# Kernel tuning notes

Hardware: AMD Instinct MI355X
Metric: run time of the kernel (lower is better)

Reference implementation:

```python
import jax, jax.numpy as jnp
import numpy as np

EPS = 1e-5
K = 20

def knn_idx(x, k):
    # x: (B, N, C). Torch computes -||xi-xj||^2 and takes topk (largest => nearest).
    xx = jnp.sum(x * x, axis=-1)                      # (B, N)
    inner = jnp.einsum('bnc,bmc->bnm', x, x)          # (B, N, N)
    neg_dist = 2.0 * inner - xx[:, :, None] - xx[:, None, :]
    return jax.lax.top_k(neg_dist, k)[1]              # (B, N, k) int32

def edge_feature(x, k):
    # x: (B, N, C) -> (B, N, k, 2C) = concat(neighbor - center, center)
    B = x.shape[0]
    idx = knn_idx(x, k)
    nb = x[jnp.arange(B)[:, None, None], idx]         # (B, N, k, C) gather
    ctr = jnp.broadcast_to(x[:, :, None, :], nb.shape)
    return jnp.concatenate([nb - ctr, ctr], axis=-1)

def batchnorm(x, gamma, beta, axes):
    # training-mode BN over `axes` (per-channel on last axis)
    m = jnp.mean(x, axis=axes, keepdims=True)
    v = jnp.var(x, axis=axes, keepdims=True)
    return (x - m) * jax.lax.rsqrt(v + EPS) * gamma + beta

def lrelu(x):
    return jnp.where(x >= 0, x, 0.2 * x)

def conv_bn_act(x, w, g, b):
    # 1x1 conv on (B, N, k, Cin) with weight (Cout, Cin), BN over (B, N, k)
    y = jnp.einsum('bnkc,oc->bnko', x, w)
    return lrelu(batchnorm(y, g, b, (0, 1, 2)))


def setup_inputs() -> dict:
    key = jax.random.key(0)
    ks = jax.random.split(key, 16)
    B, N = 4, 4096
    d = {'x': jax.random.normal(ks[0], (B, 3, N), dtype=jnp.float32)}
    d['w1'] = jax.random.normal(ks[1], (64, 6),    dtype=jnp.float32) * 0.1
    d['w2'] = jax.random.normal(ks[2], (64, 64),   dtype=jnp.float32) * 0.1
    d['w3'] = jax.random.normal(ks[3], (64, 128),  dtype=jnp.float32) * 0.1
    d['w4'] = jax.random.normal(ks[4], (64, 64),   dtype=jnp.float32) * 0.1
    d['w5'] = jax.random.normal(ks[5], (64, 128),  dtype=jnp.float32) * 0.1
    d['w6'] = jax.random.normal(ks[6], (1024, 192), dtype=jnp.float32) * 0.05
    d['wl'] = jax.random.normal(ks[7], (512, 1024), dtype=jnp.float32) * 0.05
    for i, c in zip(range(1, 8), [64, 64, 64, 64, 64, 1024, 512]):
        d[f'g{i}'] = jnp.ones((c,), jnp.float32)
        d[f'b{i}'] = jnp.zeros((c,), jnp.float32)
    return d


def reference(x, w1, w2, w3, w4, w5, w6, wl,
              g1, b1, g2, b2, g3, b3, g4, b4, g5, b5, g6, b6, g7, b7):
    p = jnp.transpose(x[:, :3, :], (0, 2, 1))         # (B, N, 3)
    # EdgeConv block 1
    e = edge_feature(p, K)                            # (B, N, k, 6)
    h = conv_bn_act(e, w1, g1, b1)
    h = conv_bn_act(h, w2, g2, b2)
    x1 = jnp.max(h, axis=2)                           # (B, N, 64)
    # EdgeConv block 2
    e = edge_feature(x1, K)                           # (B, N, k, 128)
    h = conv_bn_act(e, w3, g3, b3)
    h = conv_bn_act(h, w4, g4, b4)
    x2 = jnp.max(h, axis=2)
    # EdgeConv block 3
    e = edge_feature(x2, K)
    h = conv_bn_act(e, w5, g5, b5)
    x3 = jnp.max(h, axis=2)
    # point-wise 1x1 conv to 1024 then global max pool
    cat = jnp.concatenate([x1, x2, x3], axis=-1)      # (B, N, 192)
    h = lrelu(batchnorm(jnp.einsum('bnc,oc->bno', cat, w6), g6, b6, (0, 1)))
    g = jnp.max(h, axis=1)                            # (B, 1024)
    out = batchnorm(g @ wl.T, g7, b7, (0,))           # (B, 512)
    return out
```

## Files before the change

kernel.cpp:

```cpp
#include <hip/hip_runtime.h>

static constexpr int PB  = 4;
static constexpr int PN  = 4096;
static constexpr int PK  = 20;
static constexpr int PNT = PB*PN*PK;
#define NEGF (-3.402823466e38f)

__device__ __forceinline__ float lrelu_f(float x){ return x >= 0.f ? x : 0.2f*x; }

typedef __attribute__((ext_vector_type(8))) short short8v;
typedef __attribute__((ext_vector_type(4))) float f32x4;

__device__ __forceinline__ unsigned short f2bf(float f){
  unsigned u = __float_as_uint(f);
  unsigned r = u + 0x7FFFu + ((u>>16)&1u);
  return (unsigned short)(r>>16);
}
__device__ __forceinline__ float bf2f(unsigned short s){ return __uint_as_float(((unsigned)s)<<16); }

#define FMA4C(accv, av, bv) { accv = fmaf((av).x,(bv).x,accv); accv = fmaf((av).y,(bv).y,accv); \
                              accv = fmaf((av).z,(bv).z,accv); accv = fmaf((av).w,(bv).w,accv); }

__global__ __launch_bounds__(512) void k_knn3(const float* __restrict__ x, int* __restrict__ idxb){
  __shared__ float4 pts[PN];
  int t = threadIdx.x;
  int b = blockIdx.y;
  const float* xb = x + (size_t)b*3*PN;
  for(int i=t;i<PN;i+=512){
    float a0 = xb[i], a1 = xb[PN+i], a2 = xb[2*PN+i];
    float s = a0*a0; s = fmaf(a1,a1,s); s = fmaf(a2,a2,s);
    pts[i] = make_float4(a0,a1,a2,s);
  }
  __syncthreads();
  int lane = t & 63, w = t >> 6;
  int row = blockIdx.x*8 + w;
  float4 pi = pts[row];
  unsigned long long removed = 0ull;

#define KDIST(E) ({ float4 pj_ = pts[lane + ((E)<<6)]; \
    float dt_ = pi.x*pj_.x; dt_ = fmaf(pi.y,pj_.y,dt_); dt_ = fmaf(pi.z,pj_.z,dt_); \
    fmaf(2.f,dt_,-pi.w) - pj_.w; })

  float gv0,gv1,gv2,gv3,gv4,gv5,gv6,gv7;
  int   gi0,gi1,gi2,gi3,gi4,gi5,gi6,gi7;
#define KBUILDG(G) { float gm_=NEGF; int ge_=(G)*8; \
    _Pragma("unroll") for(int e_=(G)*8; e_<(G)*8+8; e_++){ \
      bool ok_ = ((removed >> e_) & 1ull) == 0ull; \
      float d_ = KDIST(e_); \
      bool bt_ = ok_ && (d_ > gm_); gm_ = bt_ ? d_ : gm_; ge_ = bt_ ? e_ : ge_; } \
    gv##G = gm_; gi##G = ge_; }
  KBUILDG(0) KBUILDG(1) KBUILDG(2) KBUILDG(3) KBUILDG(4) KBUILDG(5) KBUILDG(6) KBUILDG(7)

  float lmax; int le;
#define KLBEST { lmax = gv0; le = gi0; \
    if(gv1>lmax){lmax=gv1;le=gi1;} if(gv2>lmax){lmax=gv2;le=gi2;} \
    if(gv3>lmax){lmax=gv3;le=gi3;} if(gv4>lmax){lmax=gv4;le=gi4;} \
    if(gv5>lmax){lmax=gv5;le=gi5;} if(gv6>lmax){lmax=gv6;le=gi6;} \
    if(gv7>lmax){lmax=gv7;le=gi7;} }
  KLBEST

  int myidx = 0;
  for(int k=0;k<PK;k++){
    float g = lmax;
    #pragma unroll
    for(int s=32;s>=1;s>>=1) g = fmaxf(g, __shfl_xor(g, s));
    unsigned long long cand = __ballot(lmax == g);
    int jw;
    if(__popcll(cand) == 1){
      int wl = __ffsll(cand) - 1;
      int e  = __shfl(le, wl);
      jw = wl + (e<<6);
    } else {
      unsigned jj = (lmax == g) ? (unsigned)(lane + (le<<6)) : 0xFFFFFFFFu;
      #pragma unroll
      for(int s=32;s>=1;s>>=1){ unsigned o = __shfl_xor(jj, s); jj = (o < jj) ? o : jj; }
      jw = (int)jj;
    }
    if(lane == k) myidx = jw;
    if((jw & 63) == lane){
      int e = jw >> 6;
      removed |= (1ull << e);
      int q = e >> 3;
      if(q==0){ KBUILDG(0) } else if(q==1){ KBUILDG(1) }
      else if(q==2){ KBUILDG(2) } else if(q==3){ KBUILDG(3) }
      else if(q==4){ KBUILDG(4) } else if(q==5){ KBUILDG(5) }
      else if(q==6){ KBUILDG(6) } else { KBUILDG(7) }
      KLBEST
    }
  }
  if(lane < PK) idxb[((size_t)b*PN + row)*PK + lane] = myidx;
#undef KDIST
#undef KBUILDG
#undef KLBEST
}

__global__ __launch_bounds__(256) void k_dist64(const float* __restrict__ Xb, const float* __restrict__ xxb,
                                                float* __restrict__ D){
  __shared__ float Xi[128*32];
  __shared__ float Xj[128*32];
  __shared__ float xxi[128], xxj[128];
  int t = threadIdx.x;
  int p = blockIdx.x;
  int bi = (int)((65.0f - sqrtf(4225.0f - 8.0f*(float)p)) * 0.5f);
  while((bi+1)*32 - ((bi+1)*bi)/2 <= p) bi++;
  while(bi*32 - (bi*(bi-1))/2 > p) bi--;
  int bj = bi + (p - (bi*32 - (bi*(bi-1))/2));
  int i0 = bi*128, j0 = bj*128;
  int prg = t>>4, cq = t&15;
  float acc[8][8];
  #pragma unroll
  for(int pp=0;pp<8;pp++)
    #pragma unroll
    for(int oc=0;oc<8;oc++) acc[pp][oc] = 0.f;

  for(int h=0;h<2;h++){
    if(h) __syncthreads();
    #pragma unroll
    for(int k=0;k<4;k++){
      int fid = t + k*256; int row = fid>>3, c4 = fid&7;
      ((float4*)Xi)[row*8 + (c4^(row&7))] = ((const float4*)(Xb + (size_t)(i0+row)*64 + h*32))[c4];
      ((float4*)Xj)[row*8 + (c4^(row&7))] = ((const float4*)(Xb + (size_t)(j0+row)*64 + h*32))[c4];
    }
    if(h==0){
      if(t < 128) xxi[t] = xxb[i0+t];
      else        xxj[t-128] = xxb[j0+t-128];
    }
    __syncthreads();
    #pragma unroll 4
    for(int c4=0;c4<8;c4++){
      float4 a[8], bb[8];
      #pragma unroll
      for(int pp=0;pp<8;pp++){ int row = prg*8+pp; a[pp] = ((const float4*)Xi)[row*8 + (c4^(row&7))]; }
      #pragma unroll
      for(int oc=0;oc<8;oc++){ int col = cq+16*oc;  bb[oc] = ((const float4*)Xj)[col*8 + (c4^(col&7))]; }
      #pragma unroll
      for(int pp=0;pp<8;pp++)
        #pragma unroll
        for(int oc=0;oc<8;oc++) FMA4C(acc[pp][oc], a[pp], bb[oc]);
    }
  }
  #pragma unroll
  for(int pp=0;pp<8;pp++){
    int r = prg*8+pp;
    float xi2 = xxi[r];
    float* Drow = D + (size_t)(i0+r)*PN + j0;
    #pragma unroll
    for(int oc=0;oc<8;oc++){
      int c = cq + 16*oc;
      Drow[c] = fmaf(2.f, acc[pp][oc], -xi2) - xxj[c];
    }
  }
  if(bi != bj){
    #pragma unroll
    for(int oc=0;oc<8;oc++){
      int c = cq + 16*oc;
      float xj2 = xxj[c];
      float* Dcol = D + (size_t)(j0+c)*PN + i0 + prg*8;
      float4 t0, t1;
      t0.x = fmaf(2.f, acc[0][oc], -xj2) - xxi[prg*8+0];
      t0.y = fmaf(2.f, acc[1][oc], -xj2) - xxi[prg*8+1];
      t0.z = fmaf(2.f, acc[2][oc], -xj2) - xxi[prg*8+2];
      t0.w = fmaf(2.f, acc[3][oc], -xj2) - xxi[prg*8+3];
      t1.x = fmaf(2.f, acc[4][oc], -xj2) - xxi[prg*8+4];
      t1.y = fmaf(2.f, acc[5][oc], -xj2) - xxi[prg*8+5];
      t1.z = fmaf(2.f, acc[6][oc], -xj2) - xxi[prg*8+6];
      t1.w = fmaf(2.f, acc[7][oc], -xj2) - xxi[prg*8+7];
      ((float4*)Dcol)[0] = t0;
      ((float4*)Dcol)[1] = t1;
    }
  }
}

__global__ __launch_bounds__(256) void k_topk(const float* __restrict__ D, int* __restrict__ idxb){
  int t = threadIdx.x, lane = t & 63, w = t >> 6;
  int row = blockIdx.x*4 + w;
  const float4* rp = (const float4*)(D + (size_t)row*PN + lane*64);
  float v[64];
  #pragma unroll
  for(int c=0;c<16;c++){
    float4 q = rp[c];
    v[4*c+0]=q.x; v[4*c+1]=q.y; v[4*c+2]=q.z; v[4*c+3]=q.w;
  }
  float gv0,gv1,gv2,gv3,gv4,gv5,gv6,gv7;
  int   gi0,gi1,gi2,gi3,gi4,gi5,gi6,gi7;
#define TBUILDG(G) { float gm_=NEGF; int ge_=(G)*8; \
    _Pragma("unroll") for(int e_=(G)*8; e_<(G)*8+8; e_++){ \
      bool bt_ = v[e_] > gm_; gm_ = bt_ ? v[e_] : gm_; ge_ = bt_ ? e_ : ge_; } \
    gv##G = gm_; gi##G = ge_; }
#define TPOIS(G) { _Pragma("unroll") for(int e_=(G)*8; e_<(G)*8+8; e_++){ \
      if(e_ == rel) v[e_] = NEGF; } }
  TBUILDG(0) TBUILDG(1) TBUILDG(2) TBUILDG(3) TBUILDG(4) TBUILDG(5) TBUILDG(6) TBUILDG(7)
  float lmax; int li;
#define TLBEST { lmax = gv0; li = gi0; \
    if(gv1>lmax){lmax=gv1;li=gi1;} if(gv2>lmax){lmax=gv2;li=gi2;} \
    if(gv3>lmax){lmax=gv3;li=gi3;} if(gv4>lmax){lmax=gv4;li=gi4;} \
    if(gv5>lmax){lmax=gv5;li=gi5;} if(gv6>lmax){lmax=gv6;li=gi6;} \
    if(gv7>lmax){lmax=gv7;li=gi7;} }
  TLBEST
  int myidx = 0;
  for(int k=0;k<PK;k++){
    float g = lmax;
    #pragma unroll
    for(int s=32;s>=1;s>>=1) g = fmaxf(g, __shfl_xor(g, s));
    unsigned long long mask = __ballot(lmax == g);
    int wl = __ffsll((unsigned long long)mask) - 1;
    int rel = __shfl(li, wl);
    if(lane == k) myidx = wl*64 + rel;
    if(lane == wl){
      int q = rel >> 3;
      if(q==0){ TPOIS(0) TBUILDG(0) } else if(q==1){ TPOIS(1) TBUILDG(1) }
      else if(q==2){ TPOIS(2) TBUILDG(2) } else if(q==3){ TPOIS(3) TBUILDG(3) }
      else if(q==4){ TPOIS(4) TBUILDG(4) } else if(q==5){ TPOIS(5) TBUILDG(5) }
      else if(q==6){ TPOIS(6) TBUILDG(6) } else { TPOIS(7) TBUILDG(7) }
      TLBEST
    }
  }
  if(lane < PK) idxb[row*PK + lane] = myidx;
#undef TBUILDG
#undef TPOIS
#undef TLBEST
}

__global__ __launch_bounds__(256) void k_nodeUV3(const float* __restrict__ x, const float* __restrict__ w1,
                                                 float* __restrict__ U, float* __restrict__ V){
  __shared__ float ww[384];
  int t = threadIdx.x;
  for(int k=t;k<384;k+=256) ww[k] = w1[k];
  __syncthreads();
  int g = blockIdx.x*256 + t;
  int ng = g >> 6, o = g & 63;
  int b = ng >> 12, n = ng & 4095;
  const float* xb = x + (size_t)b*3*PN;
  float p0 = xb[n], p1 = xb[PN+n], p2 = xb[2*PN+n];
  const float* wr = ww + o*6;
  float u = p0*wr[0]; u = fmaf(p1,wr[1],u); u = fmaf(p2,wr[2],u);
  float vv = p0*(wr[3]-wr[0]); vv = fmaf(p1, wr[4]-wr[1], vv); vv = fmaf(p2, wr[5]-wr[2], vv);
  U[(size_t)ng*64+o] = u;
  V[(size_t)ng*64+o] = vv;
}

__global__ __launch_bounds__(256) void k_nodeUV64(const float* __restrict__ xf, const float* __restrict__ w,
                                                  float* __restrict__ U, float* __restrict__ V){
  __shared__ float xbuf[128*64];
  __shared__ float wbuf[128*64];
  int t = threadIdx.x;
  int r0 = blockIdx.x * 128;
  #pragma unroll
  for(int k=0;k<8;k++){
    int fid = t + k*256; int row = fid>>4, c4 = fid&15;
    ((float4*)xbuf)[row*16 + (c4^(row&15))] = ((const float4*)(xf + (size_t)(r0+row)*64))[c4];
    float4 wv;
    if(row < 64){
      wv = ((const float4*)(w + (size_t)row*128))[c4];
    } else {
      float4 w2v = ((const float4*)(w + (size_t)(row-64)*128 + 64))[c4];
      float4 w1v = ((const float4*)(w + (size_t)(row-64)*128))[c4];
      wv.x = w2v.x-w1v.x; wv.y = w2v.y-w1v.y; wv.z = w2v.z-w1v.z; wv.w = w2v.w-w1v.w;
    }
    ((float4*)wbuf)[row*16 + (c4^(row&15))] = wv;
  }
  __syncthreads();
  int rg = t>>4, cq = t&15;
  float acc[8][8];
  #pragma unroll
  for(int pp=0;pp<8;pp++)
    #pragma unroll
    for(int oc=0;oc<8;oc++) acc[pp][oc] = 0.f;
  #pragma unroll 4
  for(int c4=0;c4<16;c4++){
    float4 a[8], bb[8];
    #pragma unroll
    for(int pp=0;pp<8;pp++){ int row = rg*8+pp; a[pp] = ((const float4*)xbuf)[row*16 + (c4^(row&15))]; }
    #pragma unroll
    for(int oc=0;oc<8;oc++){ int col = cq+16*oc;  bb[oc] = ((const float4*)wbuf)[col*16 + (c4^(col&15))]; }
    #pragma unroll
    for(int pp=0;pp<8;pp++)
      #pragma unroll
      for(int oc=0;oc<8;oc++) FMA4C(acc[pp][oc], a[pp], bb[oc]);
  }
  #pragma unroll
  for(int pp=0;pp<8;pp++){
    int r = r0 + rg*8+pp;
    #pragma unroll
    for(int oc=0;oc<8;oc++){
      int col = cq + 16*oc;
      if(col < 64) U[(size_t)r*64 + col] = acc[pp][oc];
      else         V[(size_t)r*64 + col-64] = acc[pp][oc];
    }
  }
}

__global__ __launch_bounds__(256) void k_statUV(const float* __restrict__ U, const float* __restrict__ V,
                                                const int* __restrict__ idx, float* __restrict__ part){
  __shared__ float4 sArr[256];
  __shared__ float4 qArr[256];
  int t = threadIdx.x; int blk = blockIdx.x;
  int ch4 = t & 15, sub = t >> 4;
  int qbase = blk*640;
  float4 s = make_float4(0,0,0,0), qq = make_float4(0,0,0,0);
  for(int r=sub; r<640; r+=16){
    int q = qbase + r;
    int pt = q/PK;
    int b = pt >> 12;
    int j = idx[q];
    float4 u4 = ((const float4*)(U + (size_t)(b*PN+j)*64))[ch4];
    float4 v4 = ((const float4*)(V + (size_t)pt*64))[ch4];
    float4 y4;
    y4.x = u4.x+v4.x; y4.y = u4.y+v4.y; y4.z = u4.z+v4.z; y4.w = u4.w+v4.w;
    s.x += y4.x; s.y += y4.y; s.z += y4.z; s.w += y4.w;
    qq.x = fmaf(y4.x,y4.x,qq.x); qq.y = fmaf(y4.y,y4.y,qq.y);
    qq.z = fmaf(y4.z,y4.z,qq.z); qq.w = fmaf(y4.w,y4.w,qq.w);
  }
  sArr[t] = s; qArr[t] = qq;
  __syncthreads();
  if(t < 16){
    float4 S = make_float4(0,0,0,0), Q = make_float4(0,0,0,0);
    #pragma unroll
    for(int g=0;g<16;g++){
      float4 a = sArr[g*16 + t], b = qArr[g*16 + t];
      S.x+=a.x; S.y+=a.y; S.z+=a.z; S.w+=a.w;
      Q.x+=b.x; Q.y+=b.y; Q.z+=b.z; Q.w+=b.w;
    }
    ((float4*)(part + (size_t)blk*128))[t] = S;
    ((float4*)(part + (size_t)blk*128 + 64))[t] = Q;
  }
}

__global__ __launch_bounds__(256) void k_convAF(const float* __restrict__ U, const float* __restrict__ V,
                                                const int* __restrict__ idx, const float* __restrict__ wg,
                                                const float* __restrict__ sb, float* __restrict__ y,
                                                float* __restrict__ part){
  __shared__ short hb[2*128*64];
  __shared__ short wb[2*64*64];
  int t = threadIdx.x;
  int q0 = blockIdx.x * 128;
  #pragma unroll
  for(int k=0;k<8;k++){
    int fid = t + k*256; int row = fid>>4, c4 = fid&15;
    int q = q0 + row;
    int pt = q/PK; int b = pt>>12; int j = idx[q];
    float4 uu = ((const float4*)(U + (size_t)(b*PN+j)*64))[c4];
    float4 vv = ((const float4*)(V + (size_t)pt*64))[c4];
    float4 sc = ((const float4*)sb)[c4];
    float4 bi = ((const float4*)(sb+1024))[c4];
    float4 h;
    h.x = lrelu_f(fmaf(uu.x+vv.x, sc.x, bi.x));
    h.y = lrelu_f(fmaf(uu.y+vv.y, sc.y, bi.y));
    h.z = lrelu_f(fmaf(uu.z+vv.z, sc.z, bi.z));
    h.w = lrelu_f(fmaf(uu.w+vv.w, sc.w, bi.w));
    int base = row*64 + ((((c4>>1) ^ (row&7)))<<3) + ((c4&1)<<2);
    short4 hi4, lo4;
    hi4.x = (short)f2bf(h.x); lo4.x = (short)f2bf(h.x - bf2f((unsigned short)hi4.x));
    hi4.y = (short)f2bf(h.y); lo4.y = (short)f2bf(h.y - bf2f((unsigned short)hi4.y));
    hi4.z = (short)f2bf(h.z); lo4.z = (short)f2bf(h.z - bf2f((unsigned short)hi4.z));
    hi4.w = (short)f2bf(h.w); lo4.w = (short)f2bf(h.w - bf2f((unsigned short)hi4.w));
    *(short4*)(hb + base) = hi4;
    *(short4*)(hb + 8192 + base) = lo4;
  }
  #pragma unroll
  for(int k=0;k<4;k++){
    int fid = t + k*256; int row = fid>>4, c4 = fid&15;
    float4 wv = ((const float4*)(wg + (size_t)row*64))[c4];
    int base = row*64 + ((((c4>>1) ^ (row&7)))<<3) + ((c4&1)<<2);
    short4 hi4, lo4;
    hi4.x = (short)f2bf(wv.x); lo4.x = (short)f2bf(wv.x - bf2f((unsigned short)hi4.x));
    hi4.y = (short)f2bf(wv.y); lo4.y = (short)f2bf(wv.y - bf2f((unsigned short)hi4.y));
    hi4.z = (short)f2bf(wv.z); lo4.z = (short)f2bf(wv.z - bf2f((unsigned short)hi4.z));
    hi4.w = (short)f2bf(wv.w); lo4.w = (short)f2bf(wv.w - bf2f((unsigned short)hi4.w));
    *(short4*)(wb + base) = hi4;
    *(short4*)(wb + 4096 + base) = lo4;
  }
  __syncthreads();

  int lane = t & 63, w = t >> 6;
  int r0w = w*32;
  short8v ah[2][2], al[2][2];
  #pragma unroll
  for(int rt=0;rt<2;rt++)
    #pragma unroll
    for(int kc=0;kc<2;kc++){
      int row = r0w + rt*16 + (lane&15);
      int kb  = kc*4 + (lane>>4);
      int off = row*64 + ((kb ^ (row&7))<<3);
      ah[rt][kc] = *(const short8v*)(hb + off);
      al[rt][kc] = *(const short8v*)(hb + 8192 + off);
    }
  short8v bh[4][2], bl[4][2];
  #pragma unroll
  for(int ct=0;ct<4;ct++)
    #pragma unroll
    for(int kc=0;kc<2;kc++){
      int o   = ct*16 + (lane&15);
      int kb  = kc*4 + (lane>>4);
      int off = o*64 + ((kb ^ (o&7))<<3);
      bh[ct][kc] = *(const short8v*)(wb + off);
      bl[ct][kc] = *(const short8v*)(wb + 4096 + off);
    }

  f32x4 acc[2][4];
  #pragma unroll
  for(int rt=0;rt<2;rt++)
    #pragma unroll
    for(int ct=0;ct<4;ct++)
      acc[rt][ct] = (f32x4){0.f,0.f,0.f,0.f};

  #pragma unroll
  for(int rt=0;rt<2;rt++)
    #pragma unroll
    for(int ct=0;ct<4;ct++)
      #pragma unroll
      for(int kc=0;kc<2;kc++){
        acc[rt][ct] = __builtin_amdgcn_mfma_f32_16x16x32_bf16(ah[rt][kc], bh[ct][kc], acc[rt][ct], 0,0,0);
        acc[rt][ct] = __builtin_amdgcn_mfma_f32_16x16x32_bf16(ah[rt][kc], bl[ct][kc], acc[rt][ct], 0,0,0);
        acc[rt][ct] = __builtin_amdgcn_mfma_f32_16x16x32_bf16(al[rt][kc], bh[ct][kc], acc[rt][ct], 0,0,0);
      }

  float s_[4] = {0.f,0.f,0.f,0.f}, q_[4] = {0.f,0.f,0.f,0.f};
  #pragma unroll
  for(int rt=0;rt<2;rt++)
    #pragma unroll
    for(int ct=0;ct<4;ct++){
      int colg = ct*16 + (lane&15);
      #pragma unroll
      for(int reg=0;reg<4;reg++){
        int row = r0w + rt*16 + (lane>>4)*4 + reg;
        float val = acc[rt][ct][reg];
        y[(size_t)(q0 + row)*64 + colg] = val;
        s_[ct] += val; q_[ct] = fmaf(val, val, q_[ct]);
      }
    }

  __syncthreads();
  float* ls = (float*)wb;
  #pragma unroll
  for(int ct=0;ct<4;ct++){
    int colg = ct*16 + (lane&15);
    ls[colg*16 + (w*4 + (lane>>4))]        = s_[ct];
    ls[2048 + colg*16 + (w*4 + (lane>>4))] = q_[ct];
  }
  __syncthreads();
  if(t < 64){
    float S = 0.f, Q = 0.f;
    #pragma unroll
    for(int g=0;g<16;g++){ S += ls[t*16+g]; Q += ls[2048 + t*16+g]; }
    part[(size_t)blockIdx.x*128 + t] = S;
    part[(size_t)blockIdx.x*128 + 64 + t] = Q;
  }
}

__global__ __launch_bounds__(256) void k_red1024(const float* __restrict__ y6, float* __restrict__ part){
  int t = threadIdx.x; int blk = blockIdx.x;
  const float4* base = (const float4*)(y6 + (size_t)blk*128*1024);
  float4 s = make_float4(0,0,0,0), q = make_float4(0,0,0,0);
  for(int r=0;r<128;r++){
    float4 v = base[r*256 + t];
    s.x += v.x; s.y += v.y; s.z += v.z; s.w += v.w;
    q.x = fmaf(v.x,v.x,q.x); q.y = fmaf(v.y,v.y,q.y); q.z = fmaf(v.z,v.z,q.z); q.w = fmaf(v.w,v.w,q.w);
  }
  ((float4*)(part + (size_t)blk*2048))[t] = s;
  ((float4*)(part + (size_t)blk*2048 + 1024))[t] = q;
}

__global__ __launch_bounds__(256) void k_fin(const float* __restrict__ part, int nparts, int chn, float cnt,
                                             const float* __restrict__ gamma, const float* __restrict__ beta,
                                             float* __restrict__ sb){
  __shared__ float ls[512];
  int t = threadIdx.x;
  int chl = t & 15, sub = t >> 4;
  int ch = blockIdx.x*16 + chl;
  float S = 0.f, Q = 0.f;
  for(int p=sub; p<nparts; p+=16){
    S += part[(size_t)p*2*chn + ch];
    Q += part[(size_t)p*2*chn + chn + ch];
  }
  ls[t] = S; ls[256+t] = Q;
  __syncthreads();
  if(t < 16){
    float Sa = 0.f, Qa = 0.f;
    #pragma unroll
    for(int s=0;s<16;s++){ Sa += ls[s*16+t]; Qa += ls[256+s*16+t]; }
    int c = blockIdx.x*16 + t;
    float m  = Sa/cnt;
    float vr = Qa/cnt - m*m;
    float sc = gamma[c] * rsqrtf(vr + 1e-5f);
    sb[c] = sc; sb[1024+c] = beta[c] - m*sc;
  }
}

__global__ __launch_bounds__(256) void k_finish(const float* __restrict__ y, const float* __restrict__ sb,
                                                float* __restrict__ xo, float* __restrict__ xxo){
  __shared__ float ls[256];
  int t = threadIdx.x;
  int pt = blockIdx.x*16 + (t>>4), c4 = t&15;
  const float4* base = (const float4*)(y + (size_t)pt*20*64);
  float4 sc = ((const float4*)sb)[c4];
  float4 bi = ((const float4*)(sb+1024))[c4];
  float4 m = make_float4(NEGF,NEGF,NEGF,NEGF);
  #pragma unroll 4
  for(int k=0;k<20;k++){
    float4 v = base[k*16 + c4];
    v.x = lrelu_f(fmaf(v.x, sc.x, bi.x)); v.y = lrelu_f(fmaf(v.y, sc.y, bi.y));
    v.z = lrelu_f(fmaf(v.z, sc.z, bi.z)); v.w = lrelu_f(fmaf(v.w, sc.w, bi.w));
    m.x = fmaxf(m.x,v.x); m.y = fmaxf(m.y,v.y); m.z = fmaxf(m.z,v.z); m.w = fmaxf(m.w,v.w);
  }
  ((float4*)(xo + (size_t)pt*64))[c4] = m;
  float ss = m.x*m.x; ss = fmaf(m.y,m.y,ss); ss = fmaf(m.z,m.z,ss); ss = fmaf(m.w,m.w,ss);
  ls[t] = ss;
  __syncthreads();
  if(c4 == 0){
    float S = 0.f;
    #pragma unroll
    for(int c=0;c<16;c++) S += ls[(t & 0xF0) + c];
    xxo[pt] = S;
  }
}

__global__ __launch_bounds__(256) void k_finishUV(const float* __restrict__ U, const float* __restrict__ V,
                                                  const int* __restrict__ idx, const float* __restrict__ sb,
                                                  float* __restrict__ xo){
  int t = threadIdx.x;
  int pt = blockIdx.x*16 + (t>>4), c4 = t&15;
  int b = pt >> 12;
  float4 sc = ((const float4*)sb)[c4];
  float4 bi = ((const float4*)(sb+1024))[c4];
  float4 vv = ((const float4*)(V + (size_t)pt*64))[c4];
  float4 m = make_float4(NEGF,NEGF,NEGF,NEGF);
  const int* ip = idx + (size_t)pt*PK;
  #pragma unroll 4
  for(int k=0;k<PK;k++){
    int j = ip[k];
    float4 uu = ((const float4*)(U + (size_t)(b*PN+j)*64))[c4];
    float4 v;
    v.x = lrelu_f(fmaf(uu.x+vv.x, sc.x, bi.x)); v.y = lrelu_f(fmaf(uu.y+vv.y, sc.y, bi.y));
    v.z = lrelu_f(fmaf(uu.z+vv.z, sc.z, bi.z)); v.w = lrelu_f(fmaf(uu.w+vv.w, sc.w, bi.w));
    m.x = fmaxf(m.x,v.x); m.y = fmaxf(m.y,v.y); m.z = fmaxf(m.z,v.z); m.w = fmaxf(m.w,v.w);
  }
  ((float4*)(xo + (size_t)pt*64))[c4] = m;
}

__global__ __launch_bounds__(256) void k_gemm6(const float* __restrict__ x1, const float* __restrict__ x2,
                                               const float* __restrict__ x3, const float* __restrict__ w6,
                                               float* __restrict__ y6){
  __shared__ float cb[128*64];
  __shared__ float wb2[128*64];
  int t = threadIdx.x;
  int rb = blockIdx.x >> 3;
  int ob = blockIdx.x & 7;
  size_t r0 = (size_t)rb*128; int o0 = ob*128;
  int prg = t >> 4, cq = t & 15;
  float acc[8][8];
  #pragma unroll
  for(int pp=0;pp<8;pp++)
    #pragma unroll
    for(int oc=0;oc<8;oc++) acc[pp][oc] = 0.f;
  const float* srcs[3] = {x1, x2, x3};
  for(int ph=0; ph<3; ph++){
    __syncthreads();
    const float* src = srcs[ph];
    #pragma unroll
    for(int k=0;k<8;k++){
      int fid = t + k*256; int row = fid>>4, c4 = fid&15;
      ((float4*)cb)[row*16 + (c4^(row&15))] = ((const float4*)(src + (r0+row)*64))[c4];
      ((float4*)wb2)[row*16 + (c4^(row&15))] = ((const float4*)(w6 + (size_t)(o0+row)*192 + ph*64))[c4];
    }
    __syncthreads();
    #pragma unroll 4
    for(int c4=0;c4<16;c4++){
      float4 a[8], b8[8];
      #pragma unroll
      for(int pp=0;pp<8;pp++){ int row = prg*8+pp; a[pp] = ((const float4*)cb)[row*16 + (c4^(row&15))]; }
      #pragma unroll
      for(int oc=0;oc<8;oc++){ int och = cq + 16*oc; b8[oc] = ((const float4*)wb2)[och*16 + (c4^(och&15))]; }
      #pragma unroll
      for(int pp=0;pp<8;pp++)
        #pragma unroll
        for(int oc=0;oc<8;oc++) FMA4C(acc[pp][oc], a[pp], b8[oc]);
    }
  }
  #pragma unroll
  for(int pp=0;pp<8;pp++)
    #pragma unroll
    for(int oc=0;oc<8;oc++)
      y6[(r0 + prg*8+pp)*1024 + o0 + cq + 16*oc] = acc[pp][oc];
}

__global__ __launch_bounds__(256) void k_gmax(const float* __restrict__ y6, const float* __restrict__ sb,
                                              float* __restrict__ gpart){
  int t = threadIdx.x; int blk = blockIdx.x;
  const float4* base = (const float4*)(y6 + (size_t)blk*256*1024);
  float4 sc = ((const float4*)sb)[t];
  float4 bi = ((const float4*)(sb+1024))[t];
  float4 m = make_float4(NEGF,NEGF,NEGF,NEGF);
  for(int r=0;r<256;r++){
    float4 v = base[r*256 + t];
    v.x = lrelu_f(fmaf(v.x, sc.x, bi.x)); v.y = lrelu_f(fmaf(v.y, sc.y, bi.y));
    v.z = lrelu_f(fmaf(v.z, sc.z, bi.z)); v.w = lrelu_f(fmaf(v.w, sc.w, bi.w));
    m.x = fmaxf(m.x,v.x); m.y = fmaxf(m.y,v.y); m.z = fmaxf(m.z,v.z); m.w = fmaxf(m.w,v.w);
  }
  ((float4*)(gpart + (size_t)blk*1024))[t] = m;
}

__global__ __launch_bounds__(256) void k_gmaxfin(const float* __restrict__ gpart, float* __restrict__ g){
  int b = blockIdx.x, t = threadIdx.x;
  float4 m = make_float4(NEGF,NEGF,NEGF,NEGF);
  for(int c=0;c<16;c++){
    float4 v = ((const float4*)(gpart + ((size_t)b*16 + c)*1024))[t];
    m.x = fmaxf(m.x,v.x); m.y = fmaxf(m.y,v.y); m.z = fmaxf(m.z,v.z); m.w = fmaxf(m.w,v.w);
  }
  ((float4*)(g + (size_t)b*1024))[t] = m;
}

__global__ __launch_bounds__(256) void k_final(const float* __restrict__ g, const float* __restrict__ wl,
                                               const float* __restrict__ g7, const float* __restrict__ b7,
                                               float* __restrict__ out){
  int gt = blockIdx.x*256 + threadIdx.x;
  int o = gt >> 2, b = gt & 3;
  const float4* gb = (const float4*)(g + (size_t)b*1024);
  const float4* wr = (const float4*)(wl + (size_t)o*1024);
  float acc = 0.f;
  #pragma unroll 4
  for(int c=0;c<256;c++){
    float4 a = gb[c], w = wr[c];
    acc = fmaf(a.x,w.x,acc); acc = fmaf(a.y,w.y,acc);
    acc = fmaf(a.z,w.z,acc); acc = fmaf(a.w,w.w,acc);
  }
  float s = acc + __shfl_xor(acc, 1);
  s = s + __shfl_xor(s, 2);
  float m = s * 0.25f;
  float d = acc - m;
  float vv = d*d;
  float v2 = vv + __shfl_xor(vv, 1);
  v2 = v2 + __shfl_xor(v2, 2);
  float var = v2 * 0.25f;
  out[b*512 + o] = d * rsqrtf(var + 1e-5f) * g7[o] + b7[o];
}

extern "C" void kernel_launch(void* const* d_in, const int* in_sizes, int n_in,
                              void* d_out, int out_size, void* d_ws, size_t ws_size,
                              hipStream_t stream){
  const float* x  = (const float*)d_in[0];
  const float* w1 = (const float*)d_in[1];
  const float* w2 = (const float*)d_in[2];
  const float* w3 = (const float*)d_in[3];
  const float* w4 = (const float*)d_in[4];
  const float* w5 = (const float*)d_in[5];
  const float* w6 = (const float*)d_in[6];
  const float* wl = (const float*)d_in[7];
  const float* g1 = (const float*)d_in[8];  const float* b1 = (const float*)d_in[9];
  const float* g2 = (const float*)d_in[10]; const float* b2 = (const float*)d_in[11];
  const float* g3 = (const float*)d_in[12]; const float* b3 = (const float*)d_in[13];
  const float* g4 = (const float*)d_in[14]; const float* b4 = (const float*)d_in[15];
  const float* g5 = (const float*)d_in[16]; const float* b5 = (const float*)d_in[17];
  const float* g6 = (const float*)d_in[18]; const float* b6 = (const float*)d_in[19];
  const float* g7 = (const float*)d_in[20]; const float* b7 = (const float*)d_in[21];
  float* out = (float*)d_out;

  float* ws    = (float*)d_ws;
  float* xx    = ws;
  int*   idx   = (int*)(ws + 16384);
  float* y     = ws + 344064;
  float* Dbuf  = y;
  float* x1    = ws + 21315584;
  float* x2    = x1 + 1048576;
  float* x3    = x2 + 1048576;
  float* part  = x3 + 1048576;
  float* sb    = part + 327680;
  float* gpart = sb + 2048;
  float* g     = gpart + 65536;
  float* U     = g + 4096;
  float* V     = U + 1048576;

  k_knn3<<<dim3(512,4),512,0,stream>>>(x, idx);
  k_nodeUV3<<<4096,256,0,stream>>>(x, w1, U, V);
  k_statUV<<<512,256,0,stream>>>(U, V, idx, part);
  k_fin<<<4,256,0,stream>>>(part, 512, 64, (float)PNT, g1, b1, sb);
  k_convAF<<<2560,256,0,stream>>>(U, V, idx, w2, sb, y, part);
  k_fin<<<4,256,0,stream>>>(part, 2560, 64, (float)PNT, g2, b2, sb);
  k_finish<<<1024,256,0,stream>>>(y, sb, x1, xx);

  for(int b=0;b<PB;b++){
    k_dist64<<<528,256,0,stream>>>(x1 + (size_t)b*PN*64, xx + b*PN, Dbuf);
    k_topk<<<1024,256,0,stream>>>(Dbuf, idx + (size_t)b*PN*PK);
  }
  k_nodeUV64<<<128,256,0,stream>>>(x1, w3, U, V);
  k_statUV<<<512,256,0,stream>>>(U, V, idx, part);
  k_fin<<<4,256,0,stream>>>(part, 512, 64, (float)PNT, g3, b3, sb);
  k_convAF<<<2560,256,0,stream>>>(U, V, idx, w4, sb, y, part);
  k_fin<<<4,256,0,stream>>>(part, 2560, 64, (float)PNT, g4, b4, sb);
  k_finish<<<1024,256,0,stream>>>(y, sb, x2, xx);

  for(int b=0;b<PB;b++){
    k_dist64<<<528,256,0,stream>>>(x2 + (size_t)b*PN*64, xx + b*PN, Dbuf);
    k_topk<<<1024,256,0,stream>>>(Dbuf, idx + (size_t)b*PN*PK);
  }
  k_nodeUV64<<<128,256,0,stream>>>(x2, w5, U, V);
  k_statUV<<<512,256,0,stream>>>(U, V, idx, part);
  k_fin<<<4,256,0,stream>>>(part, 512, 64, (float)PNT, g5, b5, sb);
  k_finishUV<<<1024,256,0,stream>>>(U, V, idx, sb, x3);

  k_gemm6<<<1024,256,0,stream>>>(x1, x2, x3, w6, y);
  k_red1024<<<128,256,0,stream>>>(y, part);
  k_fin<<<64,256,0,stream>>>(part, 128, 1024, 16384.f, g6, b6, sb);
  k_gmax<<<64,256,0,stream>>>(y, sb, gpart);
  k_gmaxfin<<<4,256,0,stream>>>(gpart, g);
  k_final<<<8,256,0,stream>>>(g, wl, g7, b7, out);
}
```

Before: 1.199 ms.

## Use split-bf16 MFMA for conv6 GEMM with fused BN stats; cache kNN distances

The 16384x1024x192 pointwise GEMM now runs on bf16 MFMA, with each operand split into high and low bf16 parts and three products summed to keep near-fp32 accuracy. The per-channel sum and sum-of-squares for the following batch norm are computed in the GEMM epilogue, so the separate reduction kernel and its extra read of the output are gone. Separately, the 3-D kNN kernel precomputes all 64 distances per lane into registers and marks removed entries with -inf instead of recomputing distances from shared memory. This costs more registers and adds the bf16 split-conversion overhead when staging tiles.

```diff
diff --git a/kernel.cpp b/kernel.cpp
--- a/kernel.cpp
+++ b/kernel.cpp
@@ -35,20 +35,23 @@
   int lane = t & 63, w = t >> 6;
   int row = blockIdx.x*8 + w;
   float4 pi = pts[row];
-  unsigned long long removed = 0ull;
-
-#define KDIST(E) ({ float4 pj_ = pts[lane + ((E)<<6)]; \
-    float dt_ = pi.x*pj_.x; dt_ = fmaf(pi.y,pj_.y,dt_); dt_ = fmaf(pi.z,pj_.z,dt_); \
-    fmaf(2.f,dt_,-pi.w) - pj_.w; })
+
+  float v[64];
+  #pragma unroll
+  for(int e=0;e<64;e++){
+    float4 pj = pts[lane + (e<<6)];
+    float dt = pi.x*pj.x; dt = fmaf(pi.y,pj.y,dt); dt = fmaf(pi.z,pj.z,dt);
+    v[e] = fmaf(2.f,dt,-pi.w) - pj.w;
+  }
 
   float gv0,gv1,gv2,gv3,gv4,gv5,gv6,gv7;
   int   gi0,gi1,gi2,gi3,gi4,gi5,gi6,gi7;
 #define KBUILDG(G) { float gm_=NEGF; int ge_=(G)*8; \
     _Pragma("unroll") for(int e_=(G)*8; e_<(G)*8+8; e_++){ \
-      bool ok_ = ((removed >> e_) & 1ull) == 0ull; \
-      float d_ = KDIST(e_); \
-      bool bt_ = ok_ && (d_ > gm_); gm_ = bt_ ? d_ : gm_; ge_ = bt_ ? e_ : ge_; } \
+      bool bt_ = v[e_] > gm_; gm_ = bt_ ? v[e_] : gm_; ge_ = bt_ ? e_ : ge_; } \
     gv##G = gm_; gi##G = ge_; }
+#define KPOIS(G) { _Pragma("unroll") for(int e_=(G)*8; e_<(G)*8+8; e_++){ \
+      if(e_ == e) v[e_] = NEGF; } }
   KBUILDG(0) KBUILDG(1) KBUILDG(2) KBUILDG(3) KBUILDG(4) KBUILDG(5) KBUILDG(6) KBUILDG(7)
 
   float lmax; int le;
@@ -79,18 +82,17 @@
     if(lane == k) myidx = jw;
     if((jw & 63) == lane){
       int e = jw >> 6;
-      removed |= (1ull << e);
       int q = e >> 3;
-      if(q==0){ KBUILDG(0) } else if(q==1){ KBUILDG(1) }
-      else if(q==2){ KBUILDG(2) } else if(q==3){ KBUILDG(3) }
-      else if(q==4){ KBUILDG(4) } else if(q==5){ KBUILDG(5) }
-      else if(q==6){ KBUILDG(6) } else { KBUILDG(7) }
+      if(q==0){ KPOIS(0) KBUILDG(0) } else if(q==1){ KPOIS(1) KBUILDG(1) }
+      else if(q==2){ KPOIS(2) KBUILDG(2) } else if(q==3){ KPOIS(3) KBUILDG(3) }
+      else if(q==4){ KPOIS(4) KBUILDG(4) } else if(q==5){ KPOIS(5) KBUILDG(5) }
+      else if(q==6){ KPOIS(6) KBUILDG(6) } else { KPOIS(7) KBUILDG(7) }
       KLBEST
     }
   }
   if(lane < PK) idxb[((size_t)b*PN + row)*PK + lane] = myidx;
-#undef KDIST
 #undef KBUILDG
+#undef KPOIS
 #undef KLBEST
 }
 
@@ -448,19 +450,6 @@
   }
 }
 
-__global__ __launch_bounds__(256) void k_red1024(const float* __restrict__ y6, float* __restrict__ part){
-  int t = threadIdx.x; int blk = blockIdx.x;
-  const float4* base = (const float4*)(y6 + (size_t)blk*128*1024);
-  float4 s = make_float4(0,0,0,0), q = make_float4(0,0,0,0);
-  for(int r=0;r<128;r++){
-    float4 v = base[r*256 + t];
-    s.x += v.x; s.y += v.y; s.z += v.z; s.w += v.w;
-    q.x = fmaf(v.x,v.x,q.x); q.y = fmaf(v.y,v.y,q.y); q.z = fmaf(v.z,v.z,q.z); q.w = fmaf(v.w,v.w,q.w);
-  }
-  ((float4*)(part + (size_t)blk*2048))[t] = s;
-  ((float4*)(part + (size_t)blk*2048 + 1024))[t] = q;
-}
-
 __global__ __launch_bounds__(256) void k_fin(const float* __restrict__ part, int nparts, int chn, float cnt,
                                              const float* __restrict__ gamma, const float* __restrict__ beta,
                                              float* __restrict__ sb){
@@ -540,19 +529,20 @@
 
 __global__ __launch_bounds__(256) void k_gemm6(const float* __restrict__ x1, const float* __restrict__ x2,
                                                const float* __restrict__ x3, const float* __restrict__ w6,
-                                               float* __restrict__ y6){
-  __shared__ float cb[128*64];
-  __shared__ float wb2[128*64];
-  int t = threadIdx.x;
-  int rb = blockIdx.x >> 3;
-  int ob = blockIdx.x & 7;
+                                               float* __restrict__ y6, float* __restrict__ part){
+  __shared__ short cb[2*128*64];
+  __shared__ short wb[2*128*64];
+  int t = threadIdx.x;
+  int rb = blockIdx.x >> 3, ob = blockIdx.x & 7;
   size_t r0 = (size_t)rb*128; int o0 = ob*128;
-  int prg = t >> 4, cq = t & 15;
-  float acc[8][8];
-  #pragma unroll
-  for(int pp=0;pp<8;pp++)
-    #pragma unroll
-    for(int oc=0;oc<8;oc++) acc[pp][oc] = 0.f;
+  int lane = t & 63, w = t >> 6;
+  int r0w = w*32;
+  f32x4 acc[2][8];
+  #pragma unroll
+  for(int rt=0;rt<2;rt++)
+    #pragma unroll
+    for(int ct=0;ct<8;ct++)
+      acc[rt][ct] = (f32x4){0.f,0.f,0.f,0.f};
   const float* srcs[3] = {x1, x2, x3};
   for(int ph=0; ph<3; ph++){
     __syncthreads();
@@ -560,28 +550,86 @@
     #pragma unroll
     for(int k=0;k<8;k++){
       int fid = t + k*256; int row = fid>>4, c4 = fid&15;
-      ((float4*)cb)[row*16 + (c4^(row&15))] = ((const float4*)(src + (r0+row)*64))[c4];
-      ((float4*)wb2)[row*16 + (c4^(row&15))] = ((const float4*)(w6 + (size_t)(o0+row)*192 + ph*64))[c4];
+      float4 av = ((const float4*)(src + (r0+row)*64))[c4];
+      float4 wv = *(const float4*)(w6 + (size_t)(o0+row)*192 + ph*64 + c4*4);
+      int base = row*64 + ((((c4>>1) ^ (row&7)))<<3) + ((c4&1)<<2);
+      short4 hi4, lo4;
+      hi4.x = (short)f2bf(av.x); lo4.x = (short)f2bf(av.x - bf2f((unsigned short)hi4.x));
+      hi4.y = (short)f2bf(av.y); lo4.y = (short)f2bf(av.y - bf2f((unsigned short)hi4.y));
+      hi4.z = (short)f2bf(av.z); lo4.z = (short)f2bf(av.z - bf2f((unsigned short)hi4.z));
+      hi4.w = (short)f2bf(av.w); lo4.w = (short)f2bf(av.w - bf2f((unsigned short)hi4.w));
+      *(short4*)(cb + base) = hi4;
+      *(short4*)(cb + 8192 + base) = lo4;
+      hi4.x = (short)f2bf(wv.x); lo4.x = (short)f2bf(wv.x - bf2f((unsigned short)hi4.x));
+      hi4.y = (short)f2bf(wv.y); lo4.y = (short)f2bf(wv.y - bf2f((unsigned short)hi4.y));
+      hi4.z = (short)f2bf(wv.z); lo4.z = (short)f2bf(wv.z - bf2f((unsigned short)hi4.z));
+      hi4.w = (short)f2bf(wv.w); lo4.w = (short)f2bf(wv.w - bf2f((unsigned short)hi4.w));
+      *(short4*)(wb + base) = hi4;
+      *(short4*)(wb + 8192 + base) = lo4;
     }
     __syncthreads();
-    #pragma unroll 4
-    for(int c4=0;c4<16;c4++){
-      float4 a[8], b8[8];
-      #pragma unroll
-      for(int pp=0;pp<8;pp++){ int row = prg*8+pp; a[pp] = ((const float4*)cb)[row*16 + (c4^(row&15))]; }
-      #pragma unroll
-      for(int oc=0;oc<8;oc++){ int och = cq + 16*oc; b8[oc] = ((const float4*)wb2)[och*16 + (c4^(och&15))]; }
-      #pragma unroll
-      for(int pp=0;pp<8;pp++)
+    short8v ah[2][2], al[2][2];
+    #pragma unroll
+    for(int rt=0;rt<2;rt++)
+      #pragma unroll
+      for(int kc=0;kc<2;kc++){
+        int row = r0w + rt*16 + (lane&15);
+        int kb  = kc*4 + (lane>>4);
+        int off = row*64 + ((kb ^ (row&7))<<3);
+        ah[rt][kc] = *(const short8v*)(cb + off);
+        al[rt][kc] = *(const short8v*)(cb + 8192 + off);
+      }
+    #pragma unroll
+    for(int ct=0;ct<8;ct++){
+      short8v bh[2], bl[2];
+      #pragma unroll
+      for(int kc=0;kc<2;kc++){
+        int o   = ct*16 + (lane&15);
+        int kb  = kc*4 + (lane>>4);
+        int off = o*64 + ((kb ^ (o&7))<<3);
+        bh[kc] = *(const short8v*)(wb + off);
+        bl[kc] = *(const short8v*)(wb + 8192 + off);
+      }
+      #pragma unroll
+      for(int rt=0;rt<2;rt++)
         #pragma unroll
-        for(int oc=0;oc<8;oc++) FMA4C(acc[pp][oc], a[pp], b8[oc]);
-    }
-  }
-  #pragma unroll
-  for(int pp=0;pp<8;pp++)
-    #pragma unroll
-    for(int oc=0;oc<8;oc++)
-      y6[(r0 + prg*8+pp)*1024 + o0 + cq + 16*oc] = acc[pp][oc];
+        for(int kc=0;kc<2;kc++){
+          acc[rt][ct] = __builtin_amdgcn_mfma_f32_16x16x32_bf16(ah[rt][kc], bh[kc], acc[rt][ct], 0,0,0);
+          acc[rt][ct] = __builtin_amdgcn_mfma_f32_16x16x32_bf16(ah[rt][kc], bl[kc], acc[rt][ct], 0,0,0);
+          acc[rt][ct] = __builtin_amdgcn_mfma_f32_16x16x32_bf16(al[rt][kc], bh[kc], acc[rt][ct], 0,0,0);
+        }
+    }
+  }
+  float s_[8] = {0,0,0,0,0,0,0,0}, q_[8] = {0,0,0,0,0,0,0,0};
+  #pragma unroll
+  for(int rt=0;rt<2;rt++)
+    #pragma unroll
+    for(int ct=0;ct<8;ct++){
+      int colg = ct*16 + (lane&15);
+      #pragma unroll
+      for(int reg=0;reg<4;reg++){
+        int row = r0w + rt*16 + (lane>>4)*4 + reg;
+        float val = acc[rt][ct][reg];
+        y6[(r0 + row)*1024 + o0 + colg] = val;
+        s_[ct] += val; q_[ct] = fmaf(val, val, q_[ct]);
+      }
+    }
+  __syncthreads();
+  float* ls = (float*)wb;
+  #pragma unroll
+  for(int ct=0;ct<8;ct++){
+    int colg = ct*16 + (lane&15);
+    ls[colg*16 + (w*4 + (lane>>4))]        = s_[ct];
+    ls[2048 + colg*16 + (w*4 + (lane>>4))] = q_[ct];
+  }
+  __syncthreads();
+  if(t < 128){
+    float S = 0.f, Q = 0.f;
+    #pragma unroll
+    for(int g=0;g<16;g++){ S += ls[t*16+g]; Q += ls[2048 + t*16+g]; }
+    part[(size_t)rb*2048 + ob*128 + t] = S;
+    part[(size_t)rb*2048 + 1024 + ob*128 + t] = Q;
+  }
 }
 
 __global__ __launch_bounds__(256) void k_gmax(const float* __restrict__ y6, const float* __restrict__ sb,
@@ -698,8 +746,7 @@
   k_fin<<<4,256,0,stream>>>(part, 512, 64, (float)PNT, g5, b5, sb);
   k_finishUV<<<1024,256,0,stream>>>(U, V, idx, sb, x3);
 
-  k_gemm6<<<1024,256,0,stream>>>(x1, x2, x3, w6, y);
-  k_red1024<<<128,256,0,stream>>>(y, part);
+  k_gemm6<<<1024,256,0,stream>>>(x1, x2, x3, w6, y, part);
   k_fin<<<64,256,0,stream>>>(part, 128, 1024, 16384.f, g6, b6, sb);
   k_gmax<<<64,256,0,stream>>>(y, sb, gpart);
   k_gmaxfin<<<4,256,0,stream>>>(gpart, g);
```

After: 1.179 ms. Within noise of the previous version (-1.7%).
